# Kernel optimization log

Measured on AMD Instinct MI355X. Metric: run time of the kernel, lower is better.

Reference implementation:

```python
import jax, jax.numpy as jnp
import numpy as np

HEADS = 2
DIM_HEAD = 1
HIDDEN = HEADS * DIM_HEAD
SCALE = DIM_HEAD ** (-0.5)


def setup_inputs() -> dict:
    key = jax.random.key(0)
    ks = jax.random.split(key, 5)
    B, C, H, W, Z = 2, 64, 128, 128, 16
    return {
        "x": jax.random.normal(ks[0], (B, C, H, W, Z), dtype=jnp.float32),
        "query": jax.random.normal(ks[1], (B, C, H, W, Z), dtype=jnp.float32),
        "W_qkv": jax.random.normal(ks[2], (3 * HIDDEN, C), dtype=jnp.float32) * 0.1,
        "W_q": jax.random.normal(ks[3], (HIDDEN, C), dtype=jnp.float32) * 0.1,
        "W_out": jax.random.normal(ks[4], (C, HIDDEN), dtype=jnp.float32) * 0.1,
        "b_out": jnp.zeros((C,), dtype=jnp.float32),
    }


def reference(x, query, W_qkv, W_q, W_out, b_out):
    b, c, h, w, z = x.shape
    n = h * w * z
    xf = x.reshape(b, c, n)          # [b, c, n]
    qf = query.reshape(b, query.shape[1], n)

    # 1x1 conv3d == per-voxel linear projection; q-chunk of to_qkv is discarded
    k = jnp.einsum('bcn,oc->bon', xf, W_qkv[HIDDEN:2 * HIDDEN])   # [b, hidden, n]
    v = jnp.einsum('bcn,oc->bon', xf, W_qkv[2 * HIDDEN:3 * HIDDEN])
    q = jnp.einsum('bcn,oc->bon', qf, W_q)

    # split heads: [b, heads, dim_head, n]
    k = k.reshape(b, HEADS, DIM_HEAD, n)
    v = v.reshape(b, HEADS, DIM_HEAD, n)
    q = q.reshape(b, HEADS, DIM_HEAD, n)

    q = jax.nn.softmax(q, axis=2) * SCALE   # softmax over dim_head
    k = jax.nn.softmax(k, axis=3)           # softmax over voxels

    context = jnp.einsum('bhdn,bhen->bhde', k, v)   # [b, h, d, e]
    out = jnp.einsum('bhde,bhdn->bhen', context, q) # [b, h, e, n]
    out = out.reshape(b, HIDDEN, n)

    out = jnp.einsum('bcn,oc->bon', out, W_out) + b_out[None, :, None]
    return out.reshape(b, c, h, w, z)
```

## Files before the change

### kernel.cpp

```cpp
#include <hip/hip_runtime.h>
#include <math.h>


#define C_IN 64
#define COLS 65536
#define BLK  256
#define NB1  1024
#define CPB  64
#define GRID2 1024
#define F4_PER_BLK 8192

typedef float f32x4 __attribute__((ext_vector_type(4)));

__global__ __launch_bounds__(BLK) void k1_proj_reduce(
    const float* __restrict__ x, const float* __restrict__ Wqkv,
    float4* __restrict__ partials )
{
    __shared__ float  s_w[4][C_IN];
    __shared__ float4 s_red[4];
    const int tid = threadIdx.x;
    const int b = blockIdx.y;

    s_w[tid >> 6][tid & 63] = Wqkv[(2 + (tid >> 6)) * C_IN + (tid & 63)];
    __syncthreads();

    const int wave  = tid >> 6;
    const int lane  = tid & 63;
    const int chunk = lane >> 4;
    const int c0    = chunk << 4;
    const int col   = blockIdx.x * CPB + (wave << 4) + (lane & 15);

    const float4* xp = reinterpret_cast<const float4*>(x)
                       + (size_t)b * C_IN * COLS + (size_t)c0 * COLS + col;

    float4 kh0 = make_float4(0.f, 0.f, 0.f, 0.f);
    float4 kh1 = kh0, vh0 = kh0, vh1 = kh0;

    #pragma unroll
    for (int i = 0; i < 16; ++i) {
        float4 xv = xp[(size_t)i * COLS];
        float wk0 = s_w[0][c0 + i], wk1 = s_w[1][c0 + i];
        float wv0 = s_w[2][c0 + i], wv1 = s_w[3][c0 + i];
        kh0.x = fmaf(xv.x, wk0, kh0.x); kh0.y = fmaf(xv.y, wk0, kh0.y);
        kh0.z = fmaf(xv.z, wk0, kh0.z); kh0.w = fmaf(xv.w, wk0, kh0.w);
        kh1.x = fmaf(xv.x, wk1, kh1.x); kh1.y = fmaf(xv.y, wk1, kh1.y);
        kh1.z = fmaf(xv.z, wk1, kh1.z); kh1.w = fmaf(xv.w, wk1, kh1.w);
        vh0.x = fmaf(xv.x, wv0, vh0.x); vh0.y = fmaf(xv.y, wv0, vh0.y);
        vh0.z = fmaf(xv.z, wv0, vh0.z); vh0.w = fmaf(xv.w, wv0, vh0.w);
        vh1.x = fmaf(xv.x, wv1, vh1.x); vh1.y = fmaf(xv.y, wv1, vh1.y);
        vh1.z = fmaf(xv.z, wv1, vh1.z); vh1.w = fmaf(xv.w, wv1, vh1.w);
    }

    #pragma unroll
    for (int off = 16; off <= 32; off <<= 1) {
        kh0.x += __shfl_xor(kh0.x, off); kh0.y += __shfl_xor(kh0.y, off);
        kh0.z += __shfl_xor(kh0.z, off); kh0.w += __shfl_xor(kh0.w, off);
        kh1.x += __shfl_xor(kh1.x, off); kh1.y += __shfl_xor(kh1.y, off);
        kh1.z += __shfl_xor(kh1.z, off); kh1.w += __shfl_xor(kh1.w, off);
        vh0.x += __shfl_xor(vh0.x, off); vh0.y += __shfl_xor(vh0.y, off);
        vh0.z += __shfl_xor(vh0.z, off); vh0.w += __shfl_xor(vh0.w, off);
        vh1.x += __shfl_xor(vh1.x, off); vh1.y += __shfl_xor(vh1.y, off);
        vh1.z += __shfl_xor(vh1.z, off); vh1.w += __shfl_xor(vh1.w, off);
    }

    float s0 = 0.f, sv0 = 0.f, s1 = 0.f, sv1 = 0.f;
    float e;
    e = __expf(kh0.x); s0 += e; sv0 = fmaf(e, vh0.x, sv0);
    e = __expf(kh0.y); s0 += e; sv0 = fmaf(e, vh0.y, sv0);
    e = __expf(kh0.z); s0 += e; sv0 = fmaf(e, vh0.z, sv0);
    e = __expf(kh0.w); s0 += e; sv0 = fmaf(e, vh0.w, sv0);
    e = __expf(kh1.x); s1 += e; sv1 = fmaf(e, vh1.x, sv1);
    e = __expf(kh1.y); s1 += e; sv1 = fmaf(e, vh1.y, sv1);
    e = __expf(kh1.z); s1 += e; sv1 = fmaf(e, vh1.z, sv1);
    e = __expf(kh1.w); s1 += e; sv1 = fmaf(e, vh1.w, sv1);

    #pragma unroll
    for (int off = 1; off <= 8; off <<= 1) {
        s0  += __shfl_xor(s0,  off);
        sv0 += __shfl_xor(sv0, off);
        s1  += __shfl_xor(s1,  off);
        sv1 += __shfl_xor(sv1, off);
    }
    if (lane == 0) s_red[wave] = make_float4(s0, sv0, s1, sv1);
    __syncthreads();
    if (tid == 0) {
        float4 r0 = s_red[0], r1 = s_red[1], r2 = s_red[2], r3 = s_red[3];
        partials[(size_t)b * NB1 + blockIdx.x] =
            make_float4(r0.x + r1.x + r2.x + r3.x,
                        r0.y + r1.y + r2.y + r3.y,
                        r0.z + r1.z + r2.z + r3.z,
                        r0.w + r1.w + r2.w + r3.w);
    }
}

__global__ __launch_bounds__(BLK) void k2_combine_fill(
    const float* __restrict__ partials,
    const float* __restrict__ Wout,
    const float* __restrict__ bout,
    float* __restrict__ out)
{
    __shared__ float s_ctx[2][2];
    const int tid = threadIdx.x;
    const int wave = tid >> 6, lane = tid & 63;
    const int b = wave >> 1, h = wave & 1;

    const float2* p2 = reinterpret_cast<const float2*>(partials);
    float s = 0.f, sv = 0.f;
    #pragma unroll
    for (int i = 0; i < NB1 / 64; ++i) {
        float2 t = p2[(size_t)(b * NB1 + i * 64 + lane) * 2 + h];
        s += t.x; sv += t.y;
    }
    #pragma unroll
    for (int off = 1; off <= 32; off <<= 1) {
        s  += __shfl_xor(s,  off);
        sv += __shfl_xor(sv, off);
    }
    if (lane == 0) s_ctx[b][h] = sv / s;
    __syncthreads();

    const int row = blockIdx.x >> 3;
    const int bb = row >> 6, o = row & 63;
    const float v = fmaf(Wout[o * 2 + 0], s_ctx[bb][0],
                    fmaf(Wout[o * 2 + 1], s_ctx[bb][1], bout[o]));
    const f32x4 f4 = { v, v, v, v };

    f32x4* o4 = reinterpret_cast<f32x4*>(out);
    const size_t base = (size_t)blockIdx.x * F4_PER_BLK;
    #pragma unroll 8
    for (int k = 0; k < F4_PER_BLK / BLK; ++k)
        __builtin_nontemporal_store(f4, &o4[base + ((size_t)k << 8) + tid]);
}

extern "C" void kernel_launch(void* const* d_in, const int* in_sizes, int n_in,
                              void* d_out, int out_size, void* d_ws, size_t ws_size,
                              hipStream_t stream) {
    const float* x    = (const float*)d_in[0];
    const float* Wqkv = (const float*)d_in[2];
    const float* Wout = (const float*)d_in[4];
    const float* bout = (const float*)d_in[5];

    float4* partials = (float4*)d_ws;

    k1_proj_reduce<<<dim3(NB1, 2), BLK, 0, stream>>>(x, Wqkv, partials);
    k2_combine_fill<<<GRID2, BLK, 0, stream>>>((const float*)partials, Wout,
                                               bout, (float*)d_out);
}
```

Baseline: 53.30 us.

## Overlap batch-0 output fill with batch-1 projection in a mixed kernel

```diff
diff --git a/kernel.cpp b/kernel.cpp
--- a/kernel.cpp
+++ b/kernel.cpp
@@ -7,20 +7,17 @@
 #define BLK  256
 #define NB1  1024
 #define CPB  64
-#define GRID2 1024
-#define F4_PER_BLK 8192
+#define FILLB 512
+#define F4_PER_FILL 8192
 
 typedef float f32x4 __attribute__((ext_vector_type(4)));
 
-__global__ __launch_bounds__(BLK) void k1_proj_reduce(
+__device__ __forceinline__ void proj_reduce_body(
     const float* __restrict__ x, const float* __restrict__ Wqkv,
-    float4* __restrict__ partials )
+    float4* __restrict__ partials, const int b, const int blk,
+    float (*s_w)[C_IN], float4* s_red)
 {
-    __shared__ float  s_w[4][C_IN];
-    __shared__ float4 s_red[4];
     const int tid = threadIdx.x;
-    const int b = blockIdx.y;
-
     s_w[tid >> 6][tid & 63] = Wqkv[(2 + (tid >> 6)) * C_IN + (tid & 63)];
     __syncthreads();
 
@@ -28,7 +25,7 @@
     const int lane  = tid & 63;
     const int chunk = lane >> 4;
     const int c0    = chunk << 4;
-    const int col   = blockIdx.x * CPB + (wave << 4) + (lane & 15);
+    const int col   = blk * CPB + (wave << 4) + (lane & 15);
 
     const float4* xp = reinterpret_cast<const float4*>(x)
                        + (size_t)b * C_IN * COLS + (size_t)c0 * COLS + col;
@@ -85,7 +82,7 @@
     __syncthreads();
     if (tid == 0) {
         float4 r0 = s_red[0], r1 = s_red[1], r2 = s_red[2], r3 = s_red[3];
-        partials[(size_t)b * NB1 + blockIdx.x] =
+        partials[(size_t)b * NB1 + blk] =
             make_float4(r0.x + r1.x + r2.x + r3.x,
                         r0.y + r1.y + r2.y + r3.y,
                         r0.z + r1.z + r2.z + r3.z,
@@ -93,43 +90,76 @@
     }
 }
 
-__global__ __launch_bounds__(BLK) void k2_combine_fill(
-    const float* __restrict__ partials,
-    const float* __restrict__ Wout,
-    const float* __restrict__ bout,
-    float* __restrict__ out)
+__device__ __forceinline__ void combine_fill_body(
+    const float* __restrict__ partials, const float* __restrict__ Wout,
+    const float* __restrict__ bout, float* __restrict__ out,
+    const int bb, const int fblk, float* s_ctx )
 {
-    __shared__ float s_ctx[2][2];
     const int tid = threadIdx.x;
     const int wave = tid >> 6, lane = tid & 63;
-    const int b = wave >> 1, h = wave & 1;
 
-    const float2* p2 = reinterpret_cast<const float2*>(partials);
-    float s = 0.f, sv = 0.f;
-    #pragma unroll
-    for (int i = 0; i < NB1 / 64; ++i) {
-        float2 t = p2[(size_t)(b * NB1 + i * 64 + lane) * 2 + h];
-        s += t.x; sv += t.y;
+    if (wave < 2) {
+        const int h = wave;
+        const float2* p2 = reinterpret_cast<const float2*>(partials);
+        float s = 0.f, sv = 0.f;
+        #pragma unroll
+        for (int i = 0; i < NB1 / 64; ++i) {
+            float2 t = p2[(size_t)((bb * NB1 + i * 64 + lane) * 2 + h)];
+            s += t.x; sv += t.y;
+        }
+        #pragma unroll
+        for (int off = 1; off <= 32; off <<= 1) {
+            s  += __shfl_xor(s,  off);
+            sv += __shfl_xor(sv, off);
+        }
+        if (lane == 0) s_ctx[h] = sv / s;
     }
-    #pragma unroll
-    for (int off = 1; off <= 32; off <<= 1) {
-        s  += __shfl_xor(s,  off);
-        sv += __shfl_xor(sv, off);
-    }
-    if (lane == 0) s_ctx[b][h] = sv / s;
     __syncthreads();
 
-    const int row = blockIdx.x >> 3;
-    const int bb = row >> 6, o = row & 63;
-    const float v = fmaf(Wout[o * 2 + 0], s_ctx[bb][0],
-                    fmaf(Wout[o * 2 + 1], s_ctx[bb][1], bout[o]));
+    const int row = bb * 64 + (fblk >> 3);
+    const int o = row & 63;
+    const float v = fmaf(Wout[o * 2 + 0], s_ctx[0],
+                    fmaf(Wout[o * 2 + 1], s_ctx[1], bout[o]));
     const f32x4 f4 = { v, v, v, v };
 
     f32x4* o4 = reinterpret_cast<f32x4*>(out);
-    const size_t base = (size_t)blockIdx.x * F4_PER_BLK;
+    const size_t base = (size_t)row * COLS + (size_t)(fblk & 7) * F4_PER_FILL;
     #pragma unroll 8
-    for (int k = 0; k < F4_PER_BLK / BLK; ++k)
-        __builtin_nontemporal_store(f4, &o4[base + ((size_t)k << 8) + tid]);
+    for (int k = 0; k < F4_PER_FILL / BLK; ++k)
+        o4[base + ((size_t)k << 8) + tid] = f4;
+}
+
+__global__ __launch_bounds__(BLK) void k_proj0(
+    const float* __restrict__ x, const float* __restrict__ Wqkv,
+    float4* __restrict__ partials)
+{
+    __shared__ float  s_w[4][C_IN];
+    __shared__ float4 s_red[4];
+    proj_reduce_body(x, Wqkv, partials, 0, blockIdx.x, s_w, s_red);
+}
+
+__global__ __launch_bounds__(BLK) void k_mix(
+    const float* __restrict__ x, const float* __restrict__ Wqkv,
+    float4* __restrict__ partials, const float* __restrict__ Wout,
+    const float* __restrict__ bout, float* __restrict__ out)
+{
+    __shared__ float  s_w[4][C_IN];
+    __shared__ float4 s_red[4];
+    __shared__ float  s_ctx[2];
+    if (blockIdx.x < NB1) {
+        proj_reduce_body(x, Wqkv, partials, 1, blockIdx.x, s_w, s_red);
+    } else {
+        combine_fill_body((const float*)partials, Wout, bout, out,
+                          0, blockIdx.x - NB1, s_ctx);
+    }
+}
+
+__global__ __launch_bounds__(BLK) void k_fill1(
+    const float* __restrict__ partials, const float* __restrict__ Wout,
+    const float* __restrict__ bout, float* __restrict__ out)
+{
+    __shared__ float s_ctx[2];
+    combine_fill_body(partials, Wout, bout, out, 1, blockIdx.x, s_ctx);
 }
 
 extern "C" void kernel_launch(void* const* d_in, const int* in_sizes, int n_in,
@@ -139,10 +169,11 @@
     const float* Wqkv = (const float*)d_in[2];
     const float* Wout = (const float*)d_in[4];
     const float* bout = (const float*)d_in[5];
+    float* out = (float*)d_out;
 
     float4* partials = (float4*)d_ws;
 
-    k1_proj_reduce<<<dim3(NB1, 2), BLK, 0, stream>>>(x, Wqkv, partials);
-    k2_combine_fill<<<GRID2, BLK, 0, stream>>>((const float*)partials, Wout,
-                                               bout, (float*)d_out);
+    k_proj0<<<NB1, BLK, 0, stream>>>(x, Wqkv, partials);
+    k_mix<<<NB1 + FILLB, BLK, 0, stream>>>(x, Wqkv, partials, Wout, bout, out);
+    k_fill1<<<FILLB, BLK, 0, stream>>>((const float*)partials, Wout, bout, out);
 }
```

Result: faster. 51.75 us (-2.9%).

## Make k1 loads fully contiguous per wave and reduce channels via LDS; drop nontemporal stores

Applied to the files above, without the earlier changes.

```diff
diff --git a/kernel.cpp b/kernel.cpp
--- a/kernel.cpp
+++ b/kernel.cpp
@@ -17,30 +17,29 @@
     float4* __restrict__ partials )
 {
     __shared__ float  s_w[4][C_IN];
-    __shared__ float4 s_red[4];
+    __shared__ float4 s_part[4][4][64];
     const int tid = threadIdx.x;
     const int b = blockIdx.y;
 
     s_w[tid >> 6][tid & 63] = Wqkv[(2 + (tid >> 6)) * C_IN + (tid & 63)];
     __syncthreads();
 
-    const int wave  = tid >> 6;
-    const int lane  = tid & 63;
-    const int chunk = lane >> 4;
-    const int c0    = chunk << 4;
-    const int col   = blockIdx.x * CPB + (wave << 4) + (lane & 15);
+    const int wave = tid >> 6;
+    const int lane = tid & 63;
+    const int col  = blockIdx.x * CPB + lane;
 
     const float4* xp = reinterpret_cast<const float4*>(x)
-                       + (size_t)b * C_IN * COLS + (size_t)c0 * COLS + col;
+                       + (size_t)b * C_IN * COLS + (size_t)wave * COLS + col;
 
     float4 kh0 = make_float4(0.f, 0.f, 0.f, 0.f);
     float4 kh1 = kh0, vh0 = kh0, vh1 = kh0;
 
     #pragma unroll
     for (int i = 0; i < 16; ++i) {
-        float4 xv = xp[(size_t)i * COLS];
-        float wk0 = s_w[0][c0 + i], wk1 = s_w[1][c0 + i];
-        float wv0 = s_w[2][c0 + i], wv1 = s_w[3][c0 + i];
+        const int c = (i << 2) + wave;
+        float4 xv = xp[(size_t)(i << 2) * COLS];
+        float wk0 = s_w[0][c], wk1 = s_w[1][c];
+        float wv0 = s_w[2][c], wv1 = s_w[3][c];
         kh0.x = fmaf(xv.x, wk0, kh0.x); kh0.y = fmaf(xv.y, wk0, kh0.y);
         kh0.z = fmaf(xv.z, wk0, kh0.z); kh0.w = fmaf(xv.w, wk0, kh0.w);
         kh1.x = fmaf(xv.x, wk1, kh1.x); kh1.y = fmaf(xv.y, wk1, kh1.y);
@@ -51,45 +50,61 @@
         vh1.z = fmaf(xv.z, wv1, vh1.z); vh1.w = fmaf(xv.w, wv1, vh1.w);
     }
 
-    #pragma unroll
-    for (int off = 16; off <= 32; off <<= 1) {
-        kh0.x += __shfl_xor(kh0.x, off); kh0.y += __shfl_xor(kh0.y, off);
-        kh0.z += __shfl_xor(kh0.z, off); kh0.w += __shfl_xor(kh0.w, off);
-        kh1.x += __shfl_xor(kh1.x, off); kh1.y += __shfl_xor(kh1.y, off);
-        kh1.z += __shfl_xor(kh1.z, off); kh1.w += __shfl_xor(kh1.w, off);
-        vh0.x += __shfl_xor(vh0.x, off); vh0.y += __shfl_xor(vh0.y, off);
-        vh0.z += __shfl_xor(vh0.z, off); vh0.w += __shfl_xor(vh0.w, off);
-        vh1.x += __shfl_xor(vh1.x, off); vh1.y += __shfl_xor(vh1.y, off);
-        vh1.z += __shfl_xor(vh1.z, off); vh1.w += __shfl_xor(vh1.w, off);
-    }
+    s_part[0][wave][lane] = kh0;
+    s_part[1][wave][lane] = kh1;
+    s_part[2][wave][lane] = vh0;
+    s_part[3][wave][lane] = vh1;
+    __syncthreads();
 
-    float s0 = 0.f, sv0 = 0.f, s1 = 0.f, sv1 = 0.f;
-    float e;
-    e = __expf(kh0.x); s0 += e; sv0 = fmaf(e, vh0.x, sv0);
-    e = __expf(kh0.y); s0 += e; sv0 = fmaf(e, vh0.y, sv0);
-    e = __expf(kh0.z); s0 += e; sv0 = fmaf(e, vh0.z, sv0);
-    e = __expf(kh0.w); s0 += e; sv0 = fmaf(e, vh0.w, sv0);
-    e = __expf(kh1.x); s1 += e; sv1 = fmaf(e, vh1.x, sv1);
-    e = __expf(kh1.y); s1 += e; sv1 = fmaf(e, vh1.y, sv1);
-    e = __expf(kh1.z); s1 += e; sv1 = fmaf(e, vh1.z, sv1);
-    e = __expf(kh1.w); s1 += e; sv1 = fmaf(e, vh1.w, sv1);
+    if (tid < 64) {
+        float4 p0, p1, p2, p3;
 
-    #pragma unroll
-    for (int off = 1; off <= 8; off <<= 1) {
-        s0  += __shfl_xor(s0,  off);
-        sv0 += __shfl_xor(sv0, off);
-        s1  += __shfl_xor(s1,  off);
-        sv1 += __shfl_xor(sv1, off);
-    }
-    if (lane == 0) s_red[wave] = make_float4(s0, sv0, s1, sv1);
-    __syncthreads();
-    if (tid == 0) {
-        float4 r0 = s_red[0], r1 = s_red[1], r2 = s_red[2], r3 = s_red[3];
-        partials[(size_t)b * NB1 + blockIdx.x] =
-            make_float4(r0.x + r1.x + r2.x + r3.x,
-                        r0.y + r1.y + r2.y + r3.y,
-                        r0.z + r1.z + r2.z + r3.z,
-                        r0.w + r1.w + r2.w + r3.w);
+        p0 = s_part[0][0][tid]; p1 = s_part[0][1][tid];
+        p2 = s_part[0][2][tid]; p3 = s_part[0][3][tid];
+        float4 K0 = make_float4(p0.x + p1.x + p2.x + p3.x,
+                                p0.y + p1.y + p2.y + p3.y,
+                                p0.z + p1.z + p2.z + p3.z,
+                                p0.w + p1.w + p2.w + p3.w);
+        p0 = s_part[1][0][tid]; p1 = s_part[1][1][tid];
+        p2 = s_part[1][2][tid]; p3 = s_part[1][3][tid];
+        float4 K1 = make_float4(p0.x + p1.x + p2.x + p3.x,
+                                p0.y + p1.y + p2.y + p3.y,
+                                p0.z + p1.z + p2.z + p3.z,
+                                p0.w + p1.w + p2.w + p3.w);
+        p0 = s_part[2][0][tid]; p1 = s_part[2][1][tid];
+        p2 = s_part[2][2][tid]; p3 = s_part[2][3][tid];
+        float4 V0 = make_float4(p0.x + p1.x + p2.x + p3.x,
+                                p0.y + p1.y + p2.y + p3.y,
+                                p0.z + p1.z + p2.z + p3.z,
+                                p0.w + p1.w + p2.w + p3.w);
+        p0 = s_part[3][0][tid]; p1 = s_part[3][1][tid];
+        p2 = s_part[3][2][tid]; p3 = s_part[3][3][tid];
+        float4 V1 = make_float4(p0.x + p1.x + p2.x + p3.x,
+                                p0.y + p1.y + p2.y + p3.y,
+                                p0.z + p1.z + p2.z + p3.z,
+                                p0.w + p1.w + p2.w + p3.w);
+
+        float s0 = 0.f, sv0 = 0.f, s1 = 0.f, sv1 = 0.f;
+        float e;
+        e = __expf(K0.x); s0 += e; sv0 = fmaf(e, V0.x, sv0);
+        e = __expf(K0.y); s0 += e; sv0 = fmaf(e, V0.y, sv0);
+        e = __expf(K0.z); s0 += e; sv0 = fmaf(e, V0.z, sv0);
+        e = __expf(K0.w); s0 += e; sv0 = fmaf(e, V0.w, sv0);
+        e = __expf(K1.x); s1 += e; sv1 = fmaf(e, V1.x, sv1);
+        e = __expf(K1.y); s1 += e; sv1 = fmaf(e, V1.y, sv1);
+        e = __expf(K1.z); s1 += e; sv1 = fmaf(e, V1.z, sv1);
+        e = __expf(K1.w); s1 += e; sv1 = fmaf(e, V1.w, sv1);
+
+        #pragma unroll
+        for (int off = 1; off <= 32; off <<= 1) {
+            s0  += __shfl_xor(s0,  off);
+            sv0 += __shfl_xor(sv0, off);
+            s1  += __shfl_xor(s1,  off);
+            sv1 += __shfl_xor(sv1, off);
+        }
+        if (tid == 0)
+            partials[(size_t)b * NB1 + blockIdx.x] =
+                make_float4(s0, sv0, s1, sv1);
     }
 }
 
@@ -123,13 +138,13 @@
     const int bb = row >> 6, o = row & 63;
     const float v = fmaf(Wout[o * 2 + 0], s_ctx[bb][0],
                     fmaf(Wout[o * 2 + 1], s_ctx[bb][1], bout[o]));
-    const f32x4 f4 = { v, v, v, v };
+    const float4 f4 = make_float4(v, v, v, v);
 
-    f32x4* o4 = reinterpret_cast<f32x4*>(out);
+    float4* o4 = reinterpret_cast<float4*>(out);
     const size_t base = (size_t)blockIdx.x * F4_PER_BLK;
     #pragma unroll 8
     for (int k = 0; k < F4_PER_BLK / BLK; ++k)
-        __builtin_nontemporal_store(f4, &o4[base + ((size_t)k << 8) + tid]);
+        o4[base + ((size_t)k << 8) + tid] = f4;
 }
 
 extern "C" void kernel_launch(void* const* d_in, const int* in_sizes, int n_in,
```

Measured after the change: 49.30 us. -7.5%, faster.
